# Kernel optimization log

Hardware: AMD Instinct MI355X
Metric: run time of the kernel (lower is better)

The kernel has to match this reference:

```python
import jax, jax.numpy as jnp
import numpy as np

N, E, H = 50000, 800000, 4
IN_C, HID, OUT = 256, 64, 64
NEG_SLOPE = 0.2   # PyG GATConv default leaky_relu slope
EPS_BN = 1e-5
EPS_SM = 1e-16    # PyG softmax denominator eps


def setup_inputs() -> dict:
    key = jax.random.key(0)
    ks = jax.random.split(key, 16)
    inp = {
        "x": jax.random.normal(ks[0], (N, IN_C), jnp.float32),
        "edge_index": jax.random.randint(ks[1], (2, E), 0, N, jnp.int32),
    }
    dims = [(IN_C, HID), (HID, HID), (HID, OUT)]
    j = 2
    for l, (di, do) in enumerate(dims):
        s = 1.0 / np.sqrt(di)
        inp[f"W{l}"] = jax.random.normal(ks[j], (di, H * do), jnp.float32) * s; j += 1
        inp[f"as{l}"] = jax.random.normal(ks[j], (H, do), jnp.float32) * 0.1; j += 1
        inp[f"ad{l}"] = jax.random.normal(ks[j], (H, do), jnp.float32) * 0.1; j += 1
        inp[f"b{l}"] = jnp.zeros((do,), jnp.float32)
    for l in range(2):  # BN after all but the last conv
        inp[f"g{l}"] = jnp.ones((HID,), jnp.float32)
        inp[f"be{l}"] = jnp.zeros((HID,), jnp.float32)
    return inp


def _gat_layer(x, src, dst, W, a_src, a_dst, bias):
    """PyG GATConv, heads=H, concat=False (mean over heads), add_self_loops already in src/dst."""
    n = x.shape[0]
    C = a_src.shape[1]
    h = (x @ W).reshape(n, H, C)                      # [N,H,C]
    a_l = jnp.einsum('nhc,hc->nh', h, a_src)          # src attention term per node
    a_r = jnp.einsum('nhc,hc->nh', h, a_dst)          # dst attention term per node
    e = jax.nn.leaky_relu(a_l[src] + a_r[dst], NEG_SLOPE)   # [E',H]
    # segment softmax over incoming edges of each dst node
    m = jax.ops.segment_max(e, dst, num_segments=n)
    m = jnp.where(jnp.isfinite(m), m, 0.0)
    p = jnp.exp(e - m[dst])
    den = jax.ops.segment_sum(p, dst, num_segments=n)
    alpha = p / (den[dst] + EPS_SM)                   # [E',H]
    msg = h[src] * alpha[:, :, None]                  # [E',H,C]
    out = jax.ops.segment_sum(msg, dst, num_segments=n)
    return out.mean(axis=1) + bias                    # concat=False -> head mean, then bias


def _bn(x, g, b):
    # BatchNorm1d training-mode statistics (biased variance), eps=1e-5
    mu = x.mean(axis=0)
    var = x.var(axis=0)
    return (x - mu) * jax.lax.rsqrt(var + EPS_BN) * g + b


def reference(x, edge_index, W0, as0, ad0, b0, W1, as1, ad1, b1,
              W2, as2, ad2, b2, g0, be0, g1, be1):
    n = x.shape[0]
    loops = jnp.arange(n, dtype=edge_index.dtype)
    src = jnp.concatenate([edge_index[0], loops])
    dst = jnp.concatenate([edge_index[1], loops])

    h = _gat_layer(x, src, dst, W0, as0, ad0, b0)
    h = jax.nn.relu(_bn(h, g0, be0))                  # dropout: eval mode (identity)
    h = _gat_layer(h, src, dst, W1, as1, ad1, b1)
    h = jax.nn.relu(_bn(h, g1, be1))
    out = _gat_layer(h, src, dst, W2, as2, ad2, b2)
    return out
```

## Files before the change

kernel.cpp:

```cpp
#include <hip/hip_runtime.h>
#include <hip/hip_fp16.h>
#include <math.h>

constexpr float NEG_SLOPE = 0.2f;
constexpr float EPS_BN = 1e-5f;
constexpr float EPS_SM = 1e-16f;

typedef _Float16 half8 __attribute__((ext_vector_type(8)));
typedef float f32x4 __attribute__((ext_vector_type(4)));

__device__ __forceinline__ float lrelu(float x){ return x >= 0.f ? x : NEG_SLOPE * x; }

typedef const __attribute__((address_space(1))) unsigned int* gas_u32;
typedef __attribute__((address_space(3))) unsigned int* las_u32;

__device__ __forceinline__ void llds16(const _Float16* g, _Float16* l){
  __builtin_amdgcn_global_load_lds((gas_u32)(const void*)g, (las_u32)(void*)l, 16, 0, 0);
}

__global__ void k_prep1(const float* __restrict__ x, _Float16* __restrict__ xh, int n8,
                        const int* __restrict__ ei, int E, int* __restrict__ cnt,
                        int* __restrict__ rank,
                        const float* __restrict__ W0, const float* __restrict__ W1,
                        const float* __restrict__ W2, _Float16* __restrict__ Wt0,
                        _Float16* __restrict__ Wt1, _Float16* __restrict__ Wt2){
  int t = blockIdx.x * blockDim.x + threadIdx.x;
  if (t < n8){
    const float4* p = (const float4*)(x + (size_t)t * 8);
    float4 v0 = p[0], v1 = p[1];
    half8 h = {(_Float16)v0.x, (_Float16)v0.y, (_Float16)v0.z, (_Float16)v0.w,
               (_Float16)v1.x, (_Float16)v1.y, (_Float16)v1.z, (_Float16)v1.w};
    *(half8*)(xh + (size_t)t * 8) = h;
  }
  if (t < E) rank[t] = atomicAdd(&cnt[ei[E + t]], 1);
  if (t < 65536){
    int c = t & 255, k = t >> 8;
    Wt0[(size_t)c * 256 + k] = (_Float16)W0[(size_t)k * 256 + c];
  } else if (t < 81920){
    int u = t - 65536; int c = u & 255, k = u >> 8;
    Wt1[(size_t)c * 64 + k] = (_Float16)W1[(size_t)k * 256 + c];
  } else if (t < 98304){
    int u = t - 81920; int c = u & 255, k = u >> 8;
    Wt2[(size_t)c * 64 + k] = (_Float16)W2[(size_t)k * 256 + c];
  }
}

__global__ __launch_bounds__(256) void k_bsumscan(const int* __restrict__ cnt, int n, int chunk,
                                                  int* __restrict__ part, int* __restrict__ ptr,
                                                  int* __restrict__ tick){
  __shared__ int s[256];
  __shared__ int amLast;
  int b = blockIdx.x, t = threadIdx.x;
  int lo = b * chunk, hi = min(n, lo + chunk);
  int v = 0;
  for (int i = lo + t; i < hi; i += 256) v += cnt[i] + 1;
  s[t] = v;
  __syncthreads();
  #pragma unroll
  for (int off = 128; off > 0; off >>= 1){
    if (t < off) s[t] += s[t + off];
    __syncthreads();
  }
  if (t == 0) part[b] = s[0];
  __threadfence();
  if (t == 0) amLast = (atomicAdd(tick, 1) == (int)gridDim.x - 1) ? 1 : 0;
  __syncthreads();
  if (amLast){
    int pv = atomicAdd(&part[t], 0);
    s[t] = pv;
    __syncthreads();
    #pragma unroll
    for (int off = 1; off < 256; off <<= 1){
      int u = (t >= off) ? s[t - off] : 0;
      __syncthreads();
      s[t] += u;
      __syncthreads();
    }
    part[t] = s[t] - pv;
    if (t == 255) ptr[n] = s[255];
  }
}

__global__ __launch_bounds__(256) void k_localscan(const int* __restrict__ cnt, const int* __restrict__ part,
                                                   int n, int chunk, int* __restrict__ ptr,
                                                   int* __restrict__ csr_src){
  __shared__ int s[256];
  int b = blockIdx.x, t = threadIdx.x;
  int i = b * chunk + t;
  int c = (t < chunk && i < n) ? cnt[i] : 0;
  int v = (t < chunk && i < n) ? c + 1 : 0;
  s[t] = v;
  __syncthreads();
  #pragma unroll
  for (int off = 1; off < 256; off <<= 1){
    int u = (t >= off) ? s[t - off] : 0;
    __syncthreads();
    s[t] += u;
    __syncthreads();
  }
  if (t < chunk && i < n){
    int ex = part[b] + s[t] - v;
    ptr[i] = ex;
    csr_src[ex + c] = i;
  }
}

template<int LAYER>
__global__ __launch_bounds__(256, 2) void k_gemm(const _Float16* __restrict__ Xh,
    const float* __restrict__ Xf,
    const _Float16* __restrict__ Wt, const float* __restrict__ a_s, const float* __restrict__ a_d,
    __half* __restrict__ hb, float* __restrict__ al, float* __restrict__ ar, int nrows,
    const float* __restrict__ scale, const float* __restrict__ shift,
    const int* __restrict__ ei, int E, const int* __restrict__ rank,
    const int* __restrict__ rowptr, int* __restrict__ csr_src,
    int gemmBlocks, int N){
  constexpr int K = (LAYER == 0) ? 256 : 64;
  if (LAYER == 0 && (int)blockIdx.x >= gemmBlocks){
    int fb = (int)blockIdx.x - gemmBlocks;
    int xcd = (int)blockIdx.x & 7;
    int grp = fb >> 3;
    int ngrp = ((int)gridDim.x - gemmBlocks) >> 3;
    int nPer = N >> 3;
    int lo = xcd * nPer;
    int hi = (xcd == 7) ? N : lo + nPer;
    int stride = ngrp * 256;
    for (int e = grp * 256 + (int)threadIdx.x; e < E; e += stride){
      int dst = ei[E + e];
      if (dst >= lo && dst < hi)
        csr_src[rowptr[dst] + rank[e]] = ei[e];
    }
    return;
  }
  __shared__ _Float16 Alds[4][129][8];
  __shared__ _Float16 Blds[4][257][8];
  int tid = threadIdx.x;
  int m0 = blockIdx.x * 128;
  int w = tid >> 6, l = tid & 63;
  int lm = l & 15, lq = l >> 4;
  f32x4 acc[8][4] = {};

  for (int k0 = 0; k0 < K; k0 += 32){
    if (LAYER == 0){
      #pragma unroll
      for (int it = 0; it < 2; it++){
        int gr = m0 + it * 64 + l;
        if (gr < nrows)
          llds16(Xh + (size_t)gr * K + k0 + w * 8, &Alds[w][it * 64][0]);
      }
    } else {
      float4 sc0 = *(const float4*)(scale + k0 + w * 8);
      float4 sc1 = *(const float4*)(scale + k0 + w * 8 + 4);
      float4 sh0 = *(const float4*)(shift + k0 + w * 8);
      float4 sh1 = *(const float4*)(shift + k0 + w * 8 + 4);
      #pragma unroll
      for (int it = 0; it < 2; it++){
        int row = it * 64 + l;
        int gr = m0 + row;
        float4 v0 = make_float4(0,0,0,0), v1 = make_float4(0,0,0,0);
        if (gr < nrows){
          v0 = *(const float4*)(Xf + (size_t)gr * K + k0 + w * 8);
          v1 = *(const float4*)(Xf + (size_t)gr * K + k0 + w * 8 + 4);
        }
        v0.x = fmaxf(fmaf(v0.x, sc0.x, sh0.x), 0.f);
        v0.y = fmaxf(fmaf(v0.y, sc0.y, sh0.y), 0.f);
        v0.z = fmaxf(fmaf(v0.z, sc0.z, sh0.z), 0.f);
        v0.w = fmaxf(fmaf(v0.w, sc0.w, sh0.w), 0.f);
        v1.x = fmaxf(fmaf(v1.x, sc1.x, sh1.x), 0.f);
        v1.y = fmaxf(fmaf(v1.y, sc1.y, sh1.y), 0.f);
        v1.z = fmaxf(fmaf(v1.z, sc1.z, sh1.z), 0.f);
        v1.w = fmaxf(fmaf(v1.w, sc1.w, sh1.w), 0.f);
        half8 h = {(_Float16)v0.x, (_Float16)v0.y, (_Float16)v0.z, (_Float16)v0.w,
                   (_Float16)v1.x, (_Float16)v1.y, (_Float16)v1.z, (_Float16)v1.w};
        *(half8*)&Alds[w][row][0] = h;
      }
    }
    #pragma unroll
    for (int it = 0; it < 4; it++){
      int col = it * 64 + l;
      llds16(Wt + (size_t)col * K + k0 + w * 8, &Blds[w][it * 64][0]);
    }
    __syncthreads();
    half8 af[8];
    #pragma unroll
    for (int mf = 0; mf < 8; mf++) af[mf] = *(const half8*)&Alds[lq][mf * 16 + lm][0];
    #pragma unroll
    for (int j = 0; j < 4; j++){
      half8 bf = *(const half8*)&Blds[lq][(w * 4 + j) * 16 + lm][0];
      #pragma unroll
      for (int mf = 0; mf < 8; mf++)
        acc[mf][j] = __builtin_amdgcn_mfma_f32_16x16x32_f16(af[mf], bf, acc[mf][j], 0, 0, 0);
    }
    __syncthreads();
  }

  float asv[4], adv[4];
  #pragma unroll
  for (int j = 0; j < 4; j++){
    asv[j] = a_s[w * 64 + j * 16 + lm];
    adv[j] = a_d[w * 64 + j * 16 + lm];
  }
  #pragma unroll
  for (int mf = 0; mf < 8; mf++){
    #pragma unroll
    for (int reg = 0; reg < 4; reg++){
      float sl = acc[mf][0][reg] * asv[0] + acc[mf][1][reg] * asv[1]
               + acc[mf][2][reg] * asv[2] + acc[mf][3][reg] * asv[3];
      float sr = acc[mf][0][reg] * adv[0] + acc[mf][1][reg] * adv[1]
               + acc[mf][2][reg] * adv[2] + acc[mf][3][reg] * adv[3];
      #pragma unroll
      for (int off = 1; off < 16; off <<= 1){
        sl += __shfl_xor(sl, off);
        sr += __shfl_xor(sr, off);
      }
      int row = m0 + mf * 16 + lq * 4 + reg;
      if (lm == 0 && row < nrows){
        al[(size_t)row * 4 + w] = sl;
        ar[(size_t)row * 4 + w] = sr;
      }
      if (row < nrows){
        ushort4 pk;
        pk.x = __half_as_ushort(__float2half(acc[mf][0][reg]));
        pk.y = __half_as_ushort(__float2half(acc[mf][1][reg]));
        pk.z = __half_as_ushort(__float2half(acc[mf][2][reg]));
        pk.w = __half_as_ushort(__float2half(acc[mf][3][reg]));
        *(ushort4*)(hb + (size_t)row * 256 + w * 64 + lm * 4) = pk;
      }
    }
  }
}

__global__ __launch_bounds__(256) void k_node(const int* __restrict__ ptr,
    const int* __restrict__ csr, const __half* __restrict__ hb,
    const float* __restrict__ al, const float* __restrict__ ar,
    const float* __restrict__ bias, float* __restrict__ out, int N){
  __shared__ float4 wsm[4][64];
  __shared__ int    ssm[4][64];
  int n = (blockIdx.x * blockDim.x + threadIdx.x) >> 6;
  int lane = threadIdx.x & 63;
  int wv = threadIdx.x >> 6;
  if (n >= N) return;
  int beg = ptr[n], end = ptr[n + 1];
  int deg = end - beg;
  float4 arv = *(const float4*)(ar + (size_t)n * 4);

  if (deg <= 64){
    int idx = beg + lane;
    bool act = idx < end;
    int mye = act ? csr[idx] : 0;
    float e0 = -1e30f, e1 = -1e30f, e2 = -1e30f, e3 = -1e30f;
    if (act){
      float4 av = *(const float4*)((const char*)al + ((unsigned)mye << 4));
      e0 = lrelu(av.x + arv.x); e1 = lrelu(av.y + arv.y);
      e2 = lrelu(av.z + arv.z); e3 = lrelu(av.w + arv.w);
    }
    float m0 = e0, m1 = e1, m2 = e2, m3 = e3;
    #pragma unroll
    for (int off = 32; off > 0; off >>= 1){
      m0 = fmaxf(m0, __shfl_xor(m0, off));
      m1 = fmaxf(m1, __shfl_xor(m1, off));
      m2 = fmaxf(m2, __shfl_xor(m2, off));
      m3 = fmaxf(m3, __shfl_xor(m3, off));
    }
    float w0 = __expf(e0 - m0), w1 = __expf(e1 - m1);
    float w2 = __expf(e2 - m2), w3 = __expf(e3 - m3);
    float d0 = w0, d1 = w1, d2 = w2, d3 = w3;
    #pragma unroll
    for (int off = 32; off > 0; off >>= 1){
      d0 += __shfl_xor(d0, off);
      d1 += __shfl_xor(d1, off);
      d2 += __shfl_xor(d2, off);
      d3 += __shfl_xor(d3, off);
    }
    wsm[wv][lane] = make_float4(w0 / (d0 + EPS_SM), w1 / (d1 + EPS_SM),
                                w2 / (d2 + EPS_SM), w3 / (d3 + EPS_SM));
    ssm[wv][lane] = mye;
    __builtin_amdgcn_wave_barrier();

    int eh = lane >> 5;
    int hd = (lane >> 3) & 3;
    int c8 = lane & 7;
    unsigned choff = (unsigned)(hd * 128 + c8 * 16);
    const float* wbase = (const float*)&wsm[wv][0];
    float a0=0.f,a1=0.f,a2=0.f,a3=0.f,a4=0.f,a5=0.f,a6=0.f,a7=0.f;
    #pragma unroll 4
    for (int j = 0; j < deg; j += 2){
      int je = j + eh;
      int s = ssm[wv][je];
      float w = wbase[je * 4 + hd];
      int4 q = *(const int4*)((const char*)hb + (((unsigned)s << 9) + choff));
      const __half2* h2 = (const __half2*)&q;
      float2 f0 = __half22float2(h2[0]);
      float2 f1 = __half22float2(h2[1]);
      float2 f2 = __half22float2(h2[2]);
      float2 f3 = __half22float2(h2[3]);
      a0 = fmaf(f0.x, w, a0); a1 = fmaf(f0.y, w, a1);
      a2 = fmaf(f1.x, w, a2); a3 = fmaf(f1.y, w, a3);
      a4 = fmaf(f2.x, w, a4); a5 = fmaf(f2.y, w, a5);
      a6 = fmaf(f3.x, w, a6); a7 = fmaf(f3.y, w, a7);
    }
    #pragma unroll
    for (int off = 32; off >= 8; off >>= 1){
      a0 += __shfl_xor(a0, off); a1 += __shfl_xor(a1, off);
      a2 += __shfl_xor(a2, off); a3 += __shfl_xor(a3, off);
      a4 += __shfl_xor(a4, off); a5 += __shfl_xor(a5, off);
      a6 += __shfl_xor(a6, off); a7 += __shfl_xor(a7, off);
    }
    if (lane < 8){
      float* op = out + (size_t)n * 64 + c8 * 2;
      float2 b0 = *(const float2*)(bias + 0 * 16 + c8 * 2);
      float2 b1 = *(const float2*)(bias + 1 * 16 + c8 * 2);
      float2 b2 = *(const float2*)(bias + 2 * 16 + c8 * 2);
      float2 b3 = *(const float2*)(bias + 3 * 16 + c8 * 2);
      *(float2*)(op + 0)  = make_float2(a0 * 0.25f + b0.x, a4 * 0.25f + b0.y);
      *(float2*)(op + 16) = make_float2(a1 * 0.25f + b1.x, a5 * 0.25f + b1.y);
      *(float2*)(op + 32) = make_float2(a2 * 0.25f + b2.x, a6 * 0.25f + b2.y);
      *(float2*)(op + 48) = make_float2(a3 * 0.25f + b3.x, a7 * 0.25f + b3.y);
    }
  } else {
    int hd = lane >> 4;
    int t = lane & 15;
    const __half* hbase = hb + hd * 64 + t * 4;
    float ax = 0.f, ay = 0.f, az = 0.f, aw = 0.f;
    float m0 = -1e30f, m1 = -1e30f, m2 = -1e30f, m3 = -1e30f;
    for (int i = beg + lane; i < end; i += 64){
      int s = csr[i];
      float4 av = *(const float4*)(al + (size_t)s * 4);
      m0 = fmaxf(m0, lrelu(av.x + arv.x));
      m1 = fmaxf(m1, lrelu(av.y + arv.y));
      m2 = fmaxf(m2, lrelu(av.z + arv.z));
      m3 = fmaxf(m3, lrelu(av.w + arv.w));
    }
    #pragma unroll
    for (int off = 32; off > 0; off >>= 1){
      m0 = fmaxf(m0, __shfl_xor(m0, off));
      m1 = fmaxf(m1, __shfl_xor(m1, off));
      m2 = fmaxf(m2, __shfl_xor(m2, off));
      m3 = fmaxf(m3, __shfl_xor(m3, off));
    }
    float d0 = 0.f, d1 = 0.f, d2 = 0.f, d3 = 0.f;
    for (int i = beg + lane; i < end; i += 64){
      int s = csr[i];
      float4 av = *(const float4*)(al + (size_t)s * 4);
      d0 += __expf(lrelu(av.x + arv.x) - m0);
      d1 += __expf(lrelu(av.y + arv.y) - m1);
      d2 += __expf(lrelu(av.z + arv.z) - m2);
      d3 += __expf(lrelu(av.w + arv.w) - m3);
    }
    #pragma unroll
    for (int off = 32; off > 0; off >>= 1){
      d0 += __shfl_xor(d0, off);
      d1 += __shfl_xor(d1, off);
      d2 += __shfl_xor(d2, off);
      d3 += __shfl_xor(d3, off);
    }
    float i0 = 1.f / (d0 + EPS_SM), i1 = 1.f / (d1 + EPS_SM);
    float i2 = 1.f / (d2 + EPS_SM), i3 = 1.f / (d3 + EPS_SM);
    float arh = hd == 0 ? arv.x : hd == 1 ? arv.y : hd == 2 ? arv.z : arv.w;
    float mh  = hd == 0 ? m0 : hd == 1 ? m1 : hd == 2 ? m2 : m3;
    float ih  = hd == 0 ? i0 : hd == 1 ? i1 : hd == 2 ? i2 : i3;
    for (int i = beg; i < end; i++){
      int s = csr[i];
      float w = __expf(lrelu(al[(size_t)s * 4 + hd] + arh) - mh) * ih;
      ushort4 u = *(const ushort4*)(hbase + (size_t)s * 256);
      ax = fmaf(__half2float(__ushort_as_half(u.x)), w, ax);
      ay = fmaf(__half2float(__ushort_as_half(u.y)), w, ay);
      az = fmaf(__half2float(__ushort_as_half(u.z)), w, az);
      aw = fmaf(__half2float(__ushort_as_half(u.w)), w, aw);
    }
    #pragma unroll
    for (int off = 16; off <= 32; off <<= 1){
      ax += __shfl_xor(ax, off);
      ay += __shfl_xor(ay, off);
      az += __shfl_xor(az, off);
      aw += __shfl_xor(aw, off);
    }
    if (lane < 16){
      float* op = out + (size_t)n * 64;
      op[t]      = ax * 0.25f + bias[t];
      op[16 + t] = ay * 0.25f + bias[16 + t];
      op[32 + t] = az * 0.25f + bias[32 + t];
      op[48 + t] = aw * 0.25f + bias[48 + t];
    }
  }
}

__global__ __launch_bounds__(256) void k_bnstats(const float* __restrict__ x, int N,
                                                 float* __restrict__ gsum, float* __restrict__ gsq,
                                                 int* __restrict__ tick,
                                                 const float* __restrict__ g, const float* __restrict__ be,
                                                 float* __restrict__ scale, float* __restrict__ shift){
  int c = threadIdx.x & 63;
  int rg = threadIdx.x >> 6;
  float s = 0.f, q = 0.f;
  for (int r = blockIdx.x * 4 + rg; r < N; r += gridDim.x * 4){
    float v = x[(size_t)r * 64 + c];
    s += v; q += v * v;
  }
  __shared__ float ls[4][64], lq[4][64];
  __shared__ int amLast;
  ls[rg][c] = s; lq[rg][c] = q;
  __syncthreads();
  if (rg == 0){
    s = ls[0][c] + ls[1][c] + ls[2][c] + ls[3][c];
    q = lq[0][c] + lq[1][c] + lq[2][c] + lq[3][c];
    atomicAdd(&gsum[c], s);
    atomicAdd(&gsq[c], q);
  }
  __threadfence();
  if (threadIdx.x == 0)
    amLast = (atomicAdd(tick, 1) == (int)gridDim.x - 1) ? 1 : 0;
  __syncthreads();
  if (amLast && threadIdx.x < 64){
    float gs = atomicAdd(&gsum[c], 0.f);
    float gq = atomicAdd(&gsq[c], 0.f);
    float m = gs / (float)N;
    float v = gq / (float)N - m * m;
    float sc = g[c] * rsqrtf(v + EPS_BN);
    scale[c] = sc;
    shift[c] = be[c] - m * sc;
  }
}

extern "C" void kernel_launch(void* const* d_in, const int* in_sizes, int n_in,
                              void* d_out, int out_size, void* d_ws, size_t ws_size,
                              hipStream_t stream){
  const float* x  = (const float*)d_in[0];
  const int*   ei = (const int*)d_in[1];
  const float* W[3]  = {(const float*)d_in[2], (const float*)d_in[6],  (const float*)d_in[10]};
  const float* AS[3] = {(const float*)d_in[3], (const float*)d_in[7],  (const float*)d_in[11]};
  const float* AD[3] = {(const float*)d_in[4], (const float*)d_in[8],  (const float*)d_in[12]};
  const float* BI[3] = {(const float*)d_in[5], (const float*)d_in[9],  (const float*)d_in[13]};
  const float* G[2]  = {(const float*)d_in[14], (const float*)d_in[16]};
  const float* BE[2] = {(const float*)d_in[15], (const float*)d_in[17]};
  const int N = in_sizes[0] / 256;
  const int E = in_sizes[1] / 2;
  const int EN = E + N;

  char* wsb = (char*)d_ws;
  size_t off = 0;
  auto alloc = [&](size_t bytes) -> char* {
    char* p = wsb + off;
    off = (off + bytes + 255) & ~(size_t)255;
    return p;
  };
  int* cnt      = (int*)alloc((size_t)N * 4);
  int* rowptr   = (int*)alloc((size_t)(N + 1) * 4);
  int* part     = (int*)alloc(256 * 4);
  int* rank     = (int*)alloc((size_t)E * 4);
  int* csr      = (int*)alloc((size_t)EN * 4);
  _Float16* xh  = (_Float16*)alloc((size_t)N * 256 * 2);
  _Float16* Wt0 = (_Float16*)alloc((size_t)256 * 256 * 2);
  _Float16* Wt1 = (_Float16*)alloc((size_t)64 * 256 * 2);
  _Float16* Wt2 = (_Float16*)alloc((size_t)64 * 256 * 2);
  __half* hb    = (__half*)alloc((size_t)N * 256 * 2);
  float* al     = (float*)alloc((size_t)N * 4 * 4);
  float* ar     = (float*)alloc((size_t)N * 4 * 4);
  float* bufA   = (float*)alloc((size_t)N * 64 * 4);
  float* bn     = (float*)alloc(256 * 4);
  int*   tick   = (int*)alloc(4 * 4);
  float* murs   = (float*)alloc(128 * 4);

  const int chunk = (N + 255) / 256;
  const int n8 = N * 32;
  const int nodeGrid = (N + 3) / 4;

  hipMemsetAsync(cnt, 0, (size_t)N * 4, stream);
  hipMemsetAsync(bn, 0, 256 * 4, stream);
  hipMemsetAsync(tick, 0, 4 * 4, stream);
  k_prep1<<<(n8 + 255) / 256, 256, 0, stream>>>(x, xh, n8, ei, E, cnt, rank,
                                                W[0], W[1], W[2], Wt0, Wt1, Wt2);
  k_bsumscan<<<256, 256, 0, stream>>>(cnt, N, chunk, part, rowptr, tick + 2);
  k_localscan<<<256, 256, 0, stream>>>(cnt, part, N, chunk, rowptr, csr);

  int gemmGrid = (N + 127) / 128;
  const int FILLB = 1024;
  k_gemm<0><<<gemmGrid + FILLB, 256, 0, stream>>>(xh, nullptr, Wt0, AS[0], AD[0], hb, al, ar, N,
                                                  nullptr, nullptr, ei, E, rank, rowptr, csr,
                                                  gemmGrid, N);
  k_node<<<nodeGrid, 256, 0, stream>>>(rowptr, csr, hb, al, ar, BI[0], bufA, N);
  k_bnstats<<<128, 256, 0, stream>>>(bufA, N, bn, bn + 64, tick, G[0], BE[0], murs, murs + 64);
  k_gemm<1><<<gemmGrid, 256, 0, stream>>>(nullptr, bufA, Wt1, AS[1], AD[1], hb, al, ar, N,
                                          murs, murs + 64, nullptr, 0, nullptr, nullptr, nullptr,
                                          gemmGrid, N);
  k_node<<<nodeGrid, 256, 0, stream>>>(rowptr, csr, hb, al, ar, BI[1], bufA, N);
  k_bnstats<<<128, 256, 0, stream>>>(bufA, N, bn + 128, bn + 192, tick + 1, G[1], BE[1], murs, murs + 64);
  k_gemm<2><<<gemmGrid, 256, 0, stream>>>(nullptr, bufA, Wt2, AS[2], AD[2], hb, al, ar, N,
                                          murs, murs + 64, nullptr, 0, nullptr, nullptr, nullptr,
                                          gemmGrid, N);
  k_node<<<nodeGrid, 256, 0, stream>>>(rowptr, csr, hb, al, ar, BI[2], (float*)d_out, N);
}
```

Measured before the change: 536.5 us.

## Prefetch neighbor feature gathers in node aggregation and fold memsets into prep

In the node aggregation kernel, the first four neighbor feature rows are now loaded right after the neighbor indices are read, before the softmax reductions run. The aggregation loop keeps four register buffers and loads the row eight edges ahead, so gather latency overlaps with compute. The kernel also gets a launch-bounds occupancy hint, the BN and tick memsets move into the prep kernel to save launches, and the BN statistics grid doubles. The change raises register pressure and adds some redundant loads of row 0 for low-degree nodes.

Measured after the change: 531.6 us. No clear change (-0.9%).

```diff
diff --git a/kernel.cpp b/kernel.cpp
--- a/kernel.cpp
+++ b/kernel.cpp
@@ -23,7 +23,8 @@
                         int* __restrict__ rank,
                         const float* __restrict__ W0, const float* __restrict__ W1,
                         const float* __restrict__ W2, _Float16* __restrict__ Wt0,
-                        _Float16* __restrict__ Wt1, _Float16* __restrict__ Wt2){
+                        _Float16* __restrict__ Wt1, _Float16* __restrict__ Wt2,
+                        float* __restrict__ bn, int* __restrict__ tick){
   int t = blockIdx.x * blockDim.x + threadIdx.x;
   if (t < n8){
     const float4* p = (const float4*)(x + (size_t)t * 8);
@@ -33,6 +34,8 @@
     *(half8*)(xh + (size_t)t * 8) = h;
   }
   if (t < E) rank[t] = atomicAdd(&cnt[ei[E + t]], 1);
+  if (t < 256) bn[t] = 0.f;
+  if (t < 4) tick[t] = 0;
   if (t < 65536){
     int c = t & 255, k = t >> 8;
     Wt0[(size_t)c * 256 + k] = (_Float16)W0[(size_t)k * 256 + c];
@@ -229,7 +232,27 @@
   }
 }
 
-__global__ __launch_bounds__(256) void k_node(const int* __restrict__ ptr,
+#define AGG_STEP(QV, POFF) { \
+    int je = j + (POFF) + eh; \
+    float w = wbase[je * 4 + hd]; \
+    int4 qq = QV; \
+    int jn = je + 8; \
+    if (jn < deg){ \
+      int s = sbase[jn]; \
+      QV = *(const int4*)((const char*)hb + (((unsigned)s << 9) + choff)); \
+    } \
+    const __half2* h2 = (const __half2*)&qq; \
+    float2 f0 = __half22float2(h2[0]); \
+    float2 f1 = __half22float2(h2[1]); \
+    float2 f2 = __half22float2(h2[2]); \
+    float2 f3 = __half22float2(h2[3]); \
+    a0 = fmaf(f0.x, w, a0); a1 = fmaf(f0.y, w, a1); \
+    a2 = fmaf(f1.x, w, a2); a3 = fmaf(f1.y, w, a3); \
+    a4 = fmaf(f2.x, w, a4); a5 = fmaf(f2.y, w, a5); \
+    a6 = fmaf(f3.x, w, a6); a7 = fmaf(f3.y, w, a7); \
+  }
+
+__global__ __launch_bounds__(256, 8) void k_node(const int* __restrict__ ptr,
     const int* __restrict__ csr, const __half* __restrict__ hb,
     const float* __restrict__ al, const float* __restrict__ ar,
     const float* __restrict__ bias, float* __restrict__ out, int N){
@@ -247,12 +270,24 @@
     int idx = beg + lane;
     bool act = idx < end;
     int mye = act ? csr[idx] : 0;
+    int eh = lane >> 5;
+    int hd = (lane >> 3) & 3;
+    int c8 = lane & 7;
+    unsigned choff = (unsigned)(hd * 128 + c8 * 16);
+
     float e0 = -1e30f, e1 = -1e30f, e2 = -1e30f, e3 = -1e30f;
     if (act){
       float4 av = *(const float4*)((const char*)al + ((unsigned)mye << 4));
       e0 = lrelu(av.x + arv.x); e1 = lrelu(av.y + arv.y);
       e2 = lrelu(av.z + arv.z); e3 = lrelu(av.w + arv.w);
     }
+    int s0 = __shfl(mye, 0 + eh), s1 = __shfl(mye, 2 + eh);
+    int s2 = __shfl(mye, 4 + eh), s3 = __shfl(mye, 6 + eh);
+    int4 q0 = *(const int4*)((const char*)hb + (((unsigned)s0 << 9) + choff));
+    int4 q1 = *(const int4*)((const char*)hb + (((unsigned)s1 << 9) + choff));
+    int4 q2 = *(const int4*)((const char*)hb + (((unsigned)s2 << 9) + choff));
+    int4 q3 = *(const int4*)((const char*)hb + (((unsigned)s3 << 9) + choff));
+
     float m0 = e0, m1 = e1, m2 = e2, m3 = e3;
     #pragma unroll
     for (int off = 32; off > 0; off >>= 1){
@@ -276,27 +311,14 @@
     ssm[wv][lane] = mye;
     __builtin_amdgcn_wave_barrier();
 
-    int eh = lane >> 5;
-    int hd = (lane >> 3) & 3;
-    int c8 = lane & 7;
-    unsigned choff = (unsigned)(hd * 128 + c8 * 16);
     const float* wbase = (const float*)&wsm[wv][0];
+    const int*   sbase = &ssm[wv][0];
     float a0=0.f,a1=0.f,a2=0.f,a3=0.f,a4=0.f,a5=0.f,a6=0.f,a7=0.f;
-    #pragma unroll 4
-    for (int j = 0; j < deg; j += 2){
-      int je = j + eh;
-      int s = ssm[wv][je];
-      float w = wbase[je * 4 + hd];
-      int4 q = *(const int4*)((const char*)hb + (((unsigned)s << 9) + choff));
-      const __half2* h2 = (const __half2*)&q;
-      float2 f0 = __half22float2(h2[0]);
-      float2 f1 = __half22float2(h2[1]);
-      float2 f2 = __half22float2(h2[2]);
-      float2 f3 = __half22float2(h2[3]);
-      a0 = fmaf(f0.x, w, a0); a1 = fmaf(f0.y, w, a1);
-      a2 = fmaf(f1.x, w, a2); a3 = fmaf(f1.y, w, a3);
-      a4 = fmaf(f2.x, w, a4); a5 = fmaf(f2.y, w, a5);
-      a6 = fmaf(f3.x, w, a6); a7 = fmaf(f3.y, w, a7);
+    for (int j = 0; j < deg; j += 8){
+      AGG_STEP(q0, 0)
+      AGG_STEP(q1, 2)
+      AGG_STEP(q2, 4)
+      AGG_STEP(q3, 6)
     }
     #pragma unroll
     for (int off = 32; off >= 8; off >>= 1){
@@ -465,10 +487,8 @@
   const int nodeGrid = (N + 3) / 4;
 
   hipMemsetAsync(cnt, 0, (size_t)N * 4, stream);
-  hipMemsetAsync(bn, 0, 256 * 4, stream);
-  hipMemsetAsync(tick, 0, 4 * 4, stream);
   k_prep1<<<(n8 + 255) / 256, 256, 0, stream>>>(x, xh, n8, ei, E, cnt, rank,
-                                                W[0], W[1], W[2], Wt0, Wt1, Wt2);
+                                                W[0], W[1], W[2], Wt0, Wt1, Wt2, bn, tick);
   k_bsumscan<<<256, 256, 0, stream>>>(cnt, N, chunk, part, rowptr, tick + 2);
   k_localscan<<<256, 256, 0, stream>>>(cnt, part, N, chunk, rowptr, csr);
 
@@ -478,12 +498,12 @@
                                                   nullptr, nullptr, ei, E, rank, rowptr, csr,
                                                   gemmGrid, N);
   k_node<<<nodeGrid, 256, 0, stream>>>(rowptr, csr, hb, al, ar, BI[0], bufA, N);
-  k_bnstats<<<128, 256, 0, stream>>>(bufA, N, bn, bn + 64, tick, G[0], BE[0], murs, murs + 64);
+  k_bnstats<<<256, 256, 0, stream>>>(bufA, N, bn, bn + 64, tick, G[0], BE[0], murs, murs + 64);
   k_gemm<1><<<gemmGrid, 256, 0, stream>>>(nullptr, bufA, Wt1, AS[1], AD[1], hb, al, ar, N,
                                           murs, murs + 64, nullptr, 0, nullptr, nullptr, nullptr,
                                           gemmGrid, N);
   k_node<<<nodeGrid, 256, 0, stream>>>(rowptr, csr, hb, al, ar, BI[1], bufA, N);
-  k_bnstats<<<128, 256, 0, stream>>>(bufA, N, bn + 128, bn + 192, tick + 1, G[1], BE[1], murs, murs + 64);
+  k_bnstats<<<256, 256, 0, stream>>>(bufA, N, bn + 128, bn + 192, tick + 1, G[1], BE[1], murs, murs + 64);
   k_gemm<2><<<gemmGrid, 256, 0, stream>>>(nullptr, bufA, Wt2, AS[2], AD[2], hb, al, ar, N,
                                           murs, murs + 64, nullptr, 0, nullptr, nullptr, nullptr,
                                           gemmGrid, N);
```
